# Kernel optimization log

Hardware: AMD Instinct MI355X
Metric: run time of the kernel (lower is better)

## Reference

```python
import jax, jax.numpy as jnp
import numpy as np

B, T, TM = 4, 1024, 1500
D_MODEL, D_FFN, H, D_HEAD, D_MEM = 1024, 4096, 16, 64, 1024
EPS = 1e-5


def layernorm(x, g):
    m = jnp.mean(x, axis=-1, keepdims=True)
    xc = x - m
    v = jnp.mean(xc * xc, axis=-1, keepdims=True)
    return xc * jax.lax.rsqrt(v + EPS) * g


def setup_inputs() -> dict:
    key = jax.random.key(0)
    ks = jax.random.split(key, 12)
    s = lambda fan_in: 1.0 / np.sqrt(fan_in)
    return {
        "x": jax.random.normal(ks[0], (B, T, D_MODEL), jnp.float32),
        "encoder_output": jax.random.normal(ks[1], (B, TM, D_MEM), jnp.float32),
        "encoder_mask": jax.random.randint(ks[2], (B, TM), 0, 2).astype(bool),
        "w_qkv": jax.random.normal(ks[3], (D_MODEL, 3 * H * D_HEAD), jnp.float32) * s(D_MODEL),
        "w_o_sa": jax.random.normal(ks[4], (H * D_HEAD, D_MODEL), jnp.float32) * s(H * D_HEAD),
        "w_q": jax.random.normal(ks[5], (D_MODEL, H * D_HEAD), jnp.float32) * s(D_MODEL),
        "w_kv": jax.random.normal(ks[6], (D_MEM, 2 * H * D_HEAD), jnp.float32) * s(D_MEM),
        "w_o_xa": jax.random.normal(ks[7], (H * D_HEAD, D_MODEL), jnp.float32) * s(H * D_HEAD),
        "w_ff1": jax.random.normal(ks[8], (D_MODEL, D_FFN), jnp.float32) * s(D_MODEL),
        "w_ff2": jax.random.normal(ks[9], (D_FFN, D_MODEL), jnp.float32) * s(D_FFN),
        "g_sa": jnp.ones((D_MODEL,), jnp.float32),
        "g_xaq": jnp.ones((D_MODEL,), jnp.float32),
        "g_xam": jnp.ones((D_MEM,), jnp.float32),
        "g_ff": jnp.ones((D_MODEL,), jnp.float32),
    }


def reference(x, encoder_output, encoder_mask, w_qkv, w_o_sa, w_q, w_kv, w_o_xa,
              w_ff1, w_ff2, g_sa, g_xaq, g_xam, g_ff):
    b, t, _ = x.shape
    scale = D_HEAD ** -0.5

    # ---- causal self-attention ----
    residual = x
    xn = layernorm(x, g_sa)
    qkv = (xn @ w_qkv).reshape(b, t, 3, H, D_HEAD)
    q, k, v = qkv[:, :, 0], qkv[:, :, 1], qkv[:, :, 2]  # (B,T,H,D)
    scores = jnp.einsum('bqhd,bkhd->bhqk', q, k) * scale
    causal = jnp.tril(jnp.ones((t, t), x.dtype))
    scores = scores + (1.0 - causal) * -1e9
    attn = jax.nn.softmax(scores, axis=-1)
    sa = jnp.einsum('bhqk,bkhd->bqhd', attn, v).reshape(b, t, H * D_HEAD)
    x = residual + sa @ w_o_sa

    # ---- cross-attention ----
    residual = x
    qn = layernorm(x, g_xaq)
    mn = layernorm(encoder_output, g_xam)
    tq, tm = t, mn.shape[1]
    qx = (qn @ w_q).reshape(b, tq, H, D_HEAD)
    kvx = (mn @ w_kv).reshape(b, tm, 2, H, D_HEAD)
    kx, vx = kvx[:, :, 0], kvx[:, :, 1]
    xs = jnp.einsum('bqhd,bkhd->bhqk', qx, kx) * scale
    xs = jnp.where(encoder_mask[:, None, None, :], xs, -jnp.inf)
    xattn = jax.nn.softmax(xs, axis=-1)
    xa = jnp.einsum('bhqk,bkhd->bqhd', xattn, vx).reshape(b, tq, H * D_HEAD)
    x = residual + xa @ w_o_xa

    # ---- pointwise FFN (kernel_size=1 conv == linear) ----
    residual = x
    h = layernorm(x, g_ff)
    h = jax.nn.gelu(h @ w_ff1, approximate=True) @ w_ff2
    x = residual + h
    return (x, k, v)
```

## Files before the change

kernel.cpp:

```cpp
#include <hip/hip_runtime.h>
#include <hip/hip_bf16.h>
#include <cstdint>
#include <cstddef>


typedef __attribute__((ext_vector_type(4))) float f32x4;
typedef __attribute__((ext_vector_type(8))) short s8v;
typedef __attribute__((ext_vector_type(2))) unsigned uint2v;

#define DEVI __device__ __forceinline__

DEVI short f2bf(float f) {
  union { float f; unsigned u; } x; x.f = f;
  unsigned r = x.u + 0x7fffu + ((x.u >> 16) & 1u);
  return (short)(r >> 16);
}
DEVI unsigned cvtpk_bf2(float lo, float hi) {
  unsigned r;
  asm("v_cvt_pk_bf16_f32 %0, %1, %2" : "=v"(r) : "v"(lo), "v"(hi));
  return r;
}
DEVI float fexp2(float x) {
  float r;
  asm("v_exp_f32 %0, %1" : "=v"(r) : "v"(x));
  return r;
}
DEVI float fmax3(float a, float b, float c) {
  float r;
  asm("v_max3_f32 %0, %1, %2, %3" : "=v"(r) : "v"(a), "v"(b), "v"(c));
  return r;
}
DEVI float bpermf(int srclane, float v) {
  union { float f; int i; } x; x.f = v;
  x.i = __builtin_amdgcn_ds_bpermute(srclane << 2, x.i);
  return x.f;
}
DEVI void gload_lds16(const void* g, void* l) {
  __builtin_amdgcn_global_load_lds((const __attribute__((address_space(1))) void*)g,
                                   (__attribute__((address_space(3))) void*)l,
                                   16, 0, 0);
}

DEVI void xcd_swizzle(int& bx, int& by) {
  int gx = gridDim.x, gy = gridDim.y;
  int nxy = gx * gy, chunk = nxy >> 3;
  int orig = blockIdx.y * gx + blockIdx.x;
  int gid = (orig & 7) * chunk + (orig >> 3);
  int full = gy << 3, nfull = gx >> 3, lim = nfull * full;
  if (gid < lim) {
    int band = gid / full, r = gid - band * full;
    bx = (band << 3) + (r & 7);
    by = r >> 3;
  } else {
    int r = gid - lim, w = gx - (nfull << 3);
    bx = (nfull << 3) + r % w;
    by = r / w;
  }
}

__global__ __launch_bounds__(256) void k_prep(
    const float* __restrict__ wqkv, const float* __restrict__ wosa,
    const float* __restrict__ wq,   const float* __restrict__ wkv,
    const float* __restrict__ woxa, const float* __restrict__ wff1,
    const float* __restrict__ wff2,
    short* __restrict__ wqkv_t, short* __restrict__ wosa_t,
    short* __restrict__ wq_t,   short* __restrict__ wkv_t,
    short* __restrict__ woxa_t, short* __restrict__ wff1_t,
    short* __restrict__ wff2_t,
    const int* __restrict__ mask, unsigned long long* __restrict__ mbits) {
  int id = blockIdx.x;
  const float* w; short* wt; int K, N, tx, r;
  if (id < 3072)       { w = wqkv; wt = wqkv_t; K = 1024; N = 3072; tx = 96;  r = id; }
  else if (id < 4096)  { w = wosa; wt = wosa_t; K = 1024; N = 1024; tx = 32;  r = id - 3072; }
  else if (id < 5120)  { w = wq;   wt = wq_t;   K = 1024; N = 1024; tx = 32;  r = id - 4096; }
  else if (id < 7168)  { w = wkv;  wt = wkv_t;  K = 1024; N = 2048; tx = 64;  r = id - 5120; }
  else if (id < 8192)  { w = woxa; wt = woxa_t; K = 1024; N = 1024; tx = 32;  r = id - 7168; }
  else if (id < 12288) { w = wff1; wt = wff1_t; K = 1024; N = 4096; tx = 128; r = id - 8192; }
  else if (id < 16384) { w = wff2; wt = wff2_t; K = 4096; N = 1024; tx = 32;  r = id - 12288; }
  else {
    int t = threadIdx.x;
    if (t < 96) {
      int b = t / 24, wd = t % 24;
      unsigned long long v = 0;
      const int* mb = mask + (size_t)b * 1500;
      for (int j = 0; j < 64; j++) {
        int k = wd * 64 + j;
        if (k < 1500 && mb[k]) v |= (1ull << j);
      }
      mbits[b * 24 + wd] = v;
    }
    return;
  }
  __shared__ float tile[32][33];
  int n0 = (r % tx) * 32, k0 = (r / tx) * 32;
  int t = threadIdx.x;
  int row = t >> 3, c4 = (t & 7) * 4;
  *(f32x4*)&tile[row][c4] = *(const f32x4*)(w + (size_t)(k0 + row) * N + n0 + c4);
  __syncthreads();
  float v0 = tile[c4 + 0][row], v1 = tile[c4 + 1][row];
  float v2 = tile[c4 + 2][row], v3 = tile[c4 + 3][row];
  uint2v o = {cvtpk_bf2(v0, v1), cvtpk_bf2(v2, v3)};
  *(uint2v*)(wt + (size_t)(n0 + row) * K + k0 + c4) = o;
}

__global__ __launch_bounds__(256) void k_vtrans(
    const short* __restrict__ src, int srs, int coff,
    short* __restrict__ dst, int T, int Tp) {
  __shared__ short tile[32][72];
  int bh = blockIdx.y, b = bh >> 4, h = bh & 15;
  int t0 = blockIdx.x * 32;
  const short* sB = src + (size_t)b * T * srs + coff + h * 64;
  short* dB = dst + (size_t)bh * 64 * Tp;
  int t = threadIdx.x;
  int r = t >> 3, c = (t & 7) * 8;
  int tr = t0 + r; if (tr > T - 1) tr = T - 1;
  *(s8v*)&tile[r][c] = *(const s8v*)(sB + (size_t)tr * srs + c);
  __syncthreads();
  int d = t & 63, ch = t >> 6;
  s8v o;
#pragma unroll
  for (int j = 0; j < 8; j++) o[j] = tile[ch * 8 + j][d];
  *(s8v*)(dB + (size_t)d * Tp + t0 + ch * 8) = o;
}

__global__ __launch_bounds__(256) void k_ln2(
    const float* __restrict__ x, const float* __restrict__ gx,
    short* __restrict__ ox,
    const float* __restrict__ e, const float* __restrict__ ge,
    short* __restrict__ oe) {
  int id = blockIdx.x;
  const float* src; const float* g; short* dst; int row;
  if (id < 4096) { src = x; g = gx; dst = ox; row = id; }
  else           { src = e; g = ge; dst = oe; row = id - 4096; }
  const float* xr = src + (size_t)row * 1024;
  int t = threadIdx.x, wid = t >> 6, lane = t & 63;
  f32x4 v = ((const f32x4*)xr)[t];
  float s = v[0] + v[1] + v[2] + v[3];
#pragma unroll
  for (int m = 32; m >= 1; m >>= 1) s += __shfl_xor(s, m);
  __shared__ float red[4];
  if (lane == 0) red[wid] = s;
  __syncthreads();
  float mean = (red[0] + red[1] + red[2] + red[3]) * (1.f / 1024.f);
  float q = 0.f;
#pragma unroll
  for (int i = 0; i < 4; i++) { v[i] -= mean; q += v[i] * v[i]; }
#pragma unroll
  for (int m = 32; m >= 1; m >>= 1) q += __shfl_xor(q, m);
  __syncthreads();
  if (lane == 0) red[wid] = q;
  __syncthreads();
  float var = (red[0] + red[1] + red[2] + red[3]) * (1.f / 1024.f);
  float rs = rsqrtf(var + 1e-5f);
  f32x4 gv = ((const f32x4*)g)[t];
  uint2v w = {cvtpk_bf2(v[0] * rs * gv[0], v[1] * rs * gv[1]),
              cvtpk_bf2(v[2] * rs * gv[2], v[3] * rs * gv[3])};
  *(uint2v*)(dst + (size_t)row * 1024 + t * 4) = w;
}

__global__ __launch_bounds__(256) void k_ln(
    const float* __restrict__ x, const float* __restrict__ g,
    short* __restrict__ out) {
  int row = blockIdx.x;
  const float* xr = x + (size_t)row * 1024;
  int t = threadIdx.x, wid = t >> 6, lane = t & 63;
  f32x4 v = ((const f32x4*)xr)[t];
  float s = v[0] + v[1] + v[2] + v[3];
#pragma unroll
  for (int m = 32; m >= 1; m >>= 1) s += __shfl_xor(s, m);
  __shared__ float red[4];
  if (lane == 0) red[wid] = s;
  __syncthreads();
  float mean = (red[0] + red[1] + red[2] + red[3]) * (1.f / 1024.f);
  float q = 0.f;
#pragma unroll
  for (int i = 0; i < 4; i++) { v[i] -= mean; q += v[i] * v[i]; }
#pragma unroll
  for (int m = 32; m >= 1; m >>= 1) q += __shfl_xor(q, m);
  __syncthreads();
  if (lane == 0) red[wid] = q;
  __syncthreads();
  float var = (red[0] + red[1] + red[2] + red[3]) * (1.f / 1024.f);
  float rs = rsqrtf(var + 1e-5f);
  f32x4 gv = ((const f32x4*)g)[t];
  uint2v w = {cvtpk_bf2(v[0] * rs * gv[0], v[1] * rs * gv[1]),
              cvtpk_bf2(v[2] * rs * gv[2], v[3] * rs * gv[3])};
  *(uint2v*)(out + (size_t)row * 1024 + t * 4) = w;
}

template <bool GELU_, bool F32OUT, bool BF16OUT, bool KV>
__global__ __launch_bounds__(512) void k_gemm4(
    const short* __restrict__ A, const short* __restrict__ Bt,
    float* __restrict__ Cf, short* __restrict__ Cb,
    float* __restrict__ okv, int M, int N, int K, int lda, int ldb) {
  __shared__ short As[128 * 64];
  __shared__ short Bs[256 * 64];

  int bx, by;
  xcd_swizzle(bx, by);
  int am = bx * 128, bn = by * 256;

  int t = threadIdx.x, wid = t >> 6, lane = t & 63;
  int la = lane & 15, lb = lane >> 4;
  int wr = wid >> 2, wc = wid & 3;

  const short* gpA[2]; const short* gpB[4];
  int dofA[2], dofB[4];
#pragma unroll
  for (int l = 0; l < 2; l++) {
    int c = l * 512 + t;
    int row = c >> 3, g = c & 7;
    int ar = am + row; if (ar > M - 1) ar = M - 1;
    gpA[l] = A + (size_t)ar * lda + ((g ^ (row & 7)) << 3);
    dofA[l] = (l * 512 + wid * 64) * 8;
  }
#pragma unroll
  for (int l = 0; l < 4; l++) {
    int c = l * 512 + t;
    int row = c >> 3, g = c & 7;
    gpB[l] = Bt + (size_t)(bn + row) * ldb + ((g ^ (row & 7)) << 3);
    dofB[l] = (l * 512 + wid * 64) * 8;
  }

  int aOff[4], bOff[4];
#pragma unroll
  for (int m = 0; m < 4; m++) {
    int r = wr * 64 + m * 16 + la;
    aOff[m] = r * 64 + ((lb ^ (r & 7)) << 3);
  }
#pragma unroll
  for (int n = 0; n < 4; n++) {
    int r = wc * 64 + n * 16 + la;
    bOff[n] = r * 64 + ((lb ^ (r & 7)) << 3);
  }

  f32x4 acc[4][4];
#pragma unroll
  for (int m = 0; m < 4; m++)
#pragma unroll
    for (int n = 0; n < 4; n++) acc[m][n] = (f32x4){0.f, 0.f, 0.f, 0.f};

  int nk = K >> 6;
  for (int ks = 0; ks < nk; ++ks) {
#pragma unroll
    for (int l = 0; l < 2; l++) { gload_lds16(gpA[l], As + dofA[l]); gpA[l] += 64; }
#pragma unroll
    for (int l = 0; l < 4; l++) { gload_lds16(gpB[l], Bs + dofB[l]); gpB[l] += 64; }
    __syncthreads();
#pragma unroll
    for (int kk = 0; kk < 2; kk++) {
      s8v af[4], bfg[4];
#pragma unroll
      for (int m = 0; m < 4; m++)
        af[m] = *(const s8v*)(As + (aOff[m] ^ (kk << 5)));
#pragma unroll
      for (int n = 0; n < 4; n++)
        bfg[n] = *(const s8v*)(Bs + (bOff[n] ^ (kk << 5)));
#pragma unroll
      for (int m = 0; m < 4; m++)
#pragma unroll
        for (int n = 0; n < 4; n++)
          acc[m][n] = __builtin_amdgcn_mfma_f32_16x16x32_bf16(af[m], bfg[n], acc[m][n], 0, 0, 0);
    }
    __syncthreads();
  }

#pragma unroll
  for (int m = 0; m < 4; m++) {
    int rb = am + wr * 64 + m * 16 + lb * 4;
#pragma unroll
    for (int n = 0; n < 4; n++) {
      int col = bn + wc * 64 + n * 16 + la;
#pragma unroll
      for (int j = 0; j < 4; j++) {
        int r = rb + j;
        if (r < M) {
          float v = acc[m][n][j];
          if (GELU_) {
            float u = v;
            float y = 0.7978845608f * u * (1.f + 0.044715f * u * u);
            float e = fexp2(fminf(y * 2.88539008f, 80.f));
            float th = (e - 1.f) * __builtin_amdgcn_rcpf(e + 1.f);
            v = 0.5f * u * (1.f + th);
          }
          if (F32OUT) Cf[(size_t)r * N + col] = v;
          if (BF16OUT) Cb[(size_t)r * N + col] = f2bf(v);
          if (KV) {
            if (col >= 2048)
              okv[(size_t)4096 * 1024 + (size_t)r * 1024 + (col - 2048)] = v;
            else if (col >= 1024)
              okv[(size_t)r * 1024 + (col - 1024)] = v;
          }
        }
      }
    }
  }
}

template <bool RES, bool F32OUT, bool BF16OUT>
__global__ __launch_bounds__(256) void k_gemm5(
    const short* __restrict__ A, const short* __restrict__ Bt,
    float* __restrict__ Cf, short* __restrict__ Cb,
    const float* __restrict__ res, int M, int N, int K, int lda, int ldb) {
  __shared__ short As[128 * 64];
  __shared__ short Bs[64 * 64];

  int bx, by;
  xcd_swizzle(bx, by);
  int am = bx * 128, bn = by * 64;

  int t = threadIdx.x, wid = t >> 6, lane = t & 63;
  int la = lane & 15, lb = lane >> 4;
  int wr = wid >> 1, wc = wid & 1;

  const short* gpA[4]; const short* gpB[2];
  int dofA[4], dofB[2];
#pragma unroll
  for (int l = 0; l < 4; l++) {
    int cl = l * 256 + t;
    int row = cl >> 3, g = cl & 7;
    int ar = am + row; if (ar > M - 1) ar = M - 1;
    gpA[l] = A + (size_t)ar * lda + ((g ^ (row & 7)) << 3);
    dofA[l] = (l * 256 + wid * 64) * 8;
  }
#pragma unroll
  for (int l = 0; l < 2; l++) {
    int cl = l * 256 + t;
    int row = cl >> 3, g = cl & 7;
    gpB[l] = Bt + (size_t)(bn + row) * ldb + ((g ^ (row & 7)) << 3);
    dofB[l] = (l * 256 + wid * 64) * 8;
  }

  int aOff[4], bOff[2];
#pragma unroll
  for (int m = 0; m < 4; m++) {
    int r = wr * 64 + m * 16 + la;
    aOff[m] = r * 64 + ((lb ^ (r & 7)) << 3);
  }
#pragma unroll
  for (int n = 0; n < 2; n++) {
    int r = wc * 32 + n * 16 + la;
    bOff[n] = r * 64 + ((lb ^ (r & 7)) << 3);
  }

  f32x4 acc[4][2];
#pragma unroll
  for (int m = 0; m < 4; m++)
#pragma unroll
    for (int n = 0; n < 2; n++) acc[m][n] = (f32x4){0.f, 0.f, 0.f, 0.f};

  int nk = K >> 6;
  for (int ks = 0; ks < nk; ++ks) {
#pragma unroll
    for (int l = 0; l < 4; l++) { gload_lds16(gpA[l], As + dofA[l]); gpA[l] += 64; }
#pragma unroll
    for (int l = 0; l < 2; l++) { gload_lds16(gpB[l], Bs + dofB[l]); gpB[l] += 64; }
    __syncthreads();
#pragma unroll
    for (int kk = 0; kk < 2; kk++) {
      s8v af[4], bfg[2];
#pragma unroll
      for (int m = 0; m < 4; m++)
        af[m] = *(const s8v*)(As + (aOff[m] ^ (kk << 5)));
#pragma unroll
      for (int n = 0; n < 2; n++)
        bfg[n] = *(const s8v*)(Bs + (bOff[n] ^ (kk << 5)));
#pragma unroll
      for (int m = 0; m < 4; m++)
#pragma unroll
        for (int n = 0; n < 2; n++)
          acc[m][n] = __builtin_amdgcn_mfma_f32_16x16x32_bf16(af[m], bfg[n], acc[m][n], 0, 0, 0);
    }
    __syncthreads();
  }

#pragma unroll
  for (int m = 0; m < 4; m++) {
    int rb = am + wr * 64 + m * 16 + lb * 4;
#pragma unroll
    for (int n = 0; n < 2; n++) {
      int col = bn + wc * 32 + n * 16 + la;
#pragma unroll
      for (int j = 0; j < 4; j++) {
        int r = rb + j;
        if (r < M) {
          float v = acc[m][n][j];
          if (RES) v += res[(size_t)r * N + col];
          if (F32OUT) Cf[(size_t)r * N + col] = v;
          if (BF16OUT) Cb[(size_t)r * N + col] = f2bf(v);
        }
      }
    }
  }
}

template <bool CAUSAL>
__global__ __launch_bounds__(512) void k_attn4(
    const short* __restrict__ qbuf, int qrs,
    const short* __restrict__ kbuf, int krs,
    const short* __restrict__ vT, int vts,
    short* __restrict__ obuf, int ors,
    const unsigned long long* __restrict__ mbits, int mwords,
    int Tq, int Tk, float scale) {
  __shared__ short Ks[64 * 64];
  __shared__ short Vs[64 * 64];
  __shared__ short Ps[8 * 1024];
  int lid = blockIdx.y * gridDim.x + blockIdx.x;
  int rest = lid >> 3;
  int bh = (lid & 7) * 8 + (rest & 7);
  int qsel = rest >> 3;
  int st = CAUSAL ? (7 - qsel) : qsel;
  int b = bh >> 4, h = bh & 15;
  int t = threadIdx.x, wid = t >> 6, lane = t & 63;
  int la = lane & 15, lb = lane >> 4;
  float lscale = scale * 1.44269504f;

  const short* qB = qbuf + (size_t)b * Tq * qrs + h * 64;
  const short* kB = kbuf + (size_t)b * Tk * krs + h * 64;
  const short* vB = vT + (size_t)bh * 64 * vts;
  char* Pw = (char*)(Ps + wid * 1024);

  int sr = t >> 3, scol = (t & 7) * 8;
  int swz = sr * 64 + (scol ^ ((sr & 7) << 3));

  int q0 = st * 128 + wid * 16;
  int nkt = CAUSAL ? 2 * st + 2 : (Tk + 63) >> 6;
  int lastkt = CAUSAL ? (q0 >> 6) : nkt - 1;

  s8v qf[2];
#pragma unroll
  for (int kk = 0; kk < 2; kk++)
    qf[kk] = *(const s8v*)(qB + (size_t)(q0 + la) * qrs + kk * 32 + lb * 8);

  f32x4 accO[4];
#pragma unroll
  for (int n = 0; n < 4; n++) accO[n] = (f32x4){0.f, 0.f, 0.f, 0.f};
  float m = -1e30f, l = 0.f;

  s8v krg, vrg;
  {
    int tk = sr; if (tk > Tk - 1) tk = Tk - 1;
    krg = *(const s8v*)(kB + (size_t)tk * krs + scol);
    vrg = *(const s8v*)(vB + (size_t)sr * vts + scol);
  }

  for (int kt = 0; kt < nkt; kt++) {
    int kb0 = kt << 6;
    __syncthreads();
    *(s8v*)&Ks[swz] = krg;
    *(s8v*)&Vs[swz] = vrg;
    __syncthreads();
    if (kt + 1 < nkt) {
      int kb = kb0 + 64;
      int tk = kb + sr; if (tk > Tk - 1) tk = Tk - 1;
      krg = *(const s8v*)(kB + (size_t)tk * krs + scol);
      vrg = *(const s8v*)(vB + (size_t)sr * vts + kb + scol);
    }
    if (kt > lastkt) continue;

    bool needMask;
    unsigned long long wm = ~0ull;
    if (CAUSAL) {
      needMask = (kt == lastkt);
    } else {
      wm = mbits[(size_t)b * mwords + kt];
      needMask = (wm != ~0ull);
    }

    float sc[4][4];
    __builtin_amdgcn_s_setprio(1);
#pragma unroll
    for (int n = 0; n < 4; n++) {
      f32x4 a = (f32x4){0.f, 0.f, 0.f, 0.f};
#pragma unroll
      for (int kk = 0; kk < 2; kk++) {
        s8v kf = *(const s8v*)&Ks[(n * 16 + la) * 64 +
                                  ((kk * 32 + lb * 8) ^ ((la & 7) << 3))];
        a = __builtin_amdgcn_mfma_f32_16x16x32_bf16(kf, qf[kk], a, 0, 0, 0);
      }
      if (needMask) {
#pragma unroll
        for (int j = 0; j < 4; j++) {
          int ki = n * 16 + lb * 4 + j;
          bool ok = CAUSAL ? (kb0 + ki <= q0 + la) : (((wm >> ki) & 1ull) != 0);
          sc[n][j] = ok ? a[j] : -1e30f;
        }
      } else {
#pragma unroll
        for (int j = 0; j < 4; j++) sc[n][j] = a[j];
      }
    }
    __builtin_amdgcn_s_setprio(0);

    float rn[4];
#pragma unroll
    for (int n = 0; n < 4; n++)
      rn[n] = fmaxf(fmax3(sc[n][0], sc[n][1], sc[n][2]), sc[n][3]);
    float tm = fmaxf(fmax3(rn[0], rn[1], rn[2]), rn[3]);
    tm = fmaxf(tm, __shfl_xor(tm, 16));
    tm = fmaxf(tm, __shfl_xor(tm, 32));
    tm = fmaxf(tm * lscale, -1e4f);

    bool skip = __all(tm - m <= 10.f);
    float alpha = 1.f;
    if (!skip) {
      float mn_ = fmaxf(m, tm);
      alpha = fexp2(m - mn_);
      m = mn_;
    }
    float nm = -m;

    unsigned W[4][2];
    float ps = 0.f;
#pragma unroll
    for (int n = 0; n < 4; n++) {
      float p0 = fexp2(__builtin_fmaf(sc[n][0], lscale, nm));
      float p1 = fexp2(__builtin_fmaf(sc[n][1], lscale, nm));
      float p2 = fexp2(__builtin_fmaf(sc[n][2], lscale, nm));
      float p3 = fexp2(__builtin_fmaf(sc[n][3], lscale, nm));
      ps += (p0 + p1) + (p2 + p3);
      W[n][0] = cvtpk_bf2(p0, p1);
      W[n][1] = cvtpk_bf2(p2, p3);
    }
    ps += __shfl_xor(ps, 16);
    ps += __shfl_xor(ps, 32);
    l = l * alpha + ps;

    if (!skip) {
#pragma unroll
      for (int j = 0; j < 4; j++) {
        float aj = bpermf(lb * 20 + j, alpha);
#pragma unroll
        for (int n = 0; n < 4; n++) accO[n][j] *= aj;
      }
    }

#pragma unroll
    for (int n = 0; n < 4; n++) {
      uint2v w2 = {W[n][0], W[n][1]};
      *(uint2v*)(Pw + ((la * 128 + n * 32 + lb * 8) ^ ((la & 7) << 4))) = w2;
    }
    __builtin_amdgcn_s_setprio(1);
#pragma unroll
    for (int kk = 0; kk < 2; kk++) {
      s8v pa = *(const s8v*)(Pw + ((la * 128 + kk * 64 + lb * 16) ^ ((la & 7) << 4)));
#pragma unroll
      for (int n = 0; n < 4; n++) {
        s8v vf = *(const s8v*)&Vs[(n * 16 + la) * 64 +
                                  ((kk * 32 + lb * 8) ^ ((la & 7) << 3))];
        accO[n] = __builtin_amdgcn_mfma_f32_16x16x32_bf16(pa, vf, accO[n], 0, 0, 0);
      }
    }
    __builtin_amdgcn_s_setprio(0);
  }

#pragma unroll
  for (int j = 0; j < 4; j++) {
    float lj = bpermf(lb * 20 + j, l);
    float inv = 1.f / lj;
    int r = q0 + lb * 4 + j;
#pragma unroll
    for (int n = 0; n < 4; n++)
      obuf[(size_t)(b * Tq + r) * ors + h * 64 + n * 16 + la] = f2bf(accO[n][j] * inv);
  }
}

extern "C" void kernel_launch(void* const* d_in, const int* in_sizes, int n_in,
                              void* d_out, int out_size, void* d_ws, size_t ws_size,
                              hipStream_t stream) {
  (void)in_sizes; (void)n_in; (void)out_size; (void)ws_size;
  const float* x      = (const float*)d_in[0];
  const float* enc    = (const float*)d_in[1];
  const int*   mask   = (const int*)d_in[2];
  const float* w_qkv  = (const float*)d_in[3];
  const float* w_o_sa = (const float*)d_in[4];
  const float* w_q    = (const float*)d_in[5];
  const float* w_kv   = (const float*)d_in[6];
  const float* w_o_xa = (const float*)d_in[7];
  const float* w_ff1  = (const float*)d_in[8];
  const float* w_ff2  = (const float*)d_in[9];
  const float* g_sa   = (const float*)d_in[10];
  const float* g_xaq  = (const float*)d_in[11];
  const float* g_xam  = (const float*)d_in[12];
  const float* g_ff   = (const float*)d_in[13];

  float* out_x = (float*)d_out;
  float* out_k = out_x + (size_t)4096 * 1024;

  char* ws = (char*)d_ws;
  size_t off = 0;
  auto alloc = [&](size_t bytes) -> void* {
    void* p = ws + off;
    off += (bytes + 255) & ~(size_t)255;
    return p;
  };
  short* wqkv_t = (short*)alloc((size_t)3072 * 1024 * 2);
  short* wosa_t = (short*)alloc((size_t)1024 * 1024 * 2);
  short* wq_t   = (short*)alloc((size_t)1024 * 1024 * 2);
  short* wkv_t  = (short*)alloc((size_t)2048 * 1024 * 2);
  short* woxa_t = (short*)alloc((size_t)1024 * 1024 * 2);
  short* wff1_t = (short*)alloc((size_t)4096 * 1024 * 2);
  short* wff2_t = (short*)alloc((size_t)1024 * 4096 * 2);
  short* xn     = (short*)alloc((size_t)4096 * 1024 * 2);
  short* qkv_b  = (short*)alloc((size_t)4096 * 3072 * 2);
  short* sa_b   = (short*)alloc((size_t)4096 * 1024 * 2);
  float* x1     = (float*)alloc((size_t)4096 * 1024 * 4);
  short* qn     = (short*)alloc((size_t)4096 * 1024 * 2);
  short* mn     = (short*)alloc((size_t)6000 * 1024 * 2);
  short* qx_b   = (short*)alloc((size_t)4096 * 1024 * 2);
  short* kvx_b  = (short*)alloc((size_t)6000 * 2048 * 2);
  short* xa_b   = (short*)alloc((size_t)4096 * 1024 * 2);
  float* x2     = (float*)alloc((size_t)4096 * 1024 * 4);
  short* hn     = (short*)alloc((size_t)4096 * 1024 * 2);
  short* h1     = (short*)alloc((size_t)4096 * 4096 * 2);
  unsigned long long* mbits = (unsigned long long*)alloc(4 * 24 * 8);

  short* vTsa = xn;
  short* vTxa = h1;

  k_prep<<<16385, 256, 0, stream>>>(
      w_qkv, w_o_sa, w_q, w_kv, w_o_xa, w_ff1, w_ff2,
      wqkv_t, wosa_t, wq_t, wkv_t, woxa_t, wff1_t, wff2_t, mask, mbits);
  k_ln2<<<10096, 256, 0, stream>>>(x, g_sa, xn, enc, g_xam, mn);

  k_gemm4<false, false, true, true><<<dim3(32, 12), 512, 0, stream>>>(
      xn, wqkv_t, nullptr, qkv_b, out_k, 4096, 3072, 1024, 1024, 1024);
  k_vtrans<<<dim3(32, 64), 256, 0, stream>>>(qkv_b, 3072, 2048, vTsa, 1024, 1024);
  k_attn4<true><<<dim3(8, 64), 512, 0, stream>>>(
      qkv_b, 3072, qkv_b + 1024, 3072, vTsa, 1024,
      sa_b, 1024, nullptr, 0, 1024, 1024, 0.125f);
  k_gemm5<true, true, false><<<dim3(32, 16), 256, 0, stream>>>(
      sa_b, wosa_t, x1, nullptr, x, 4096, 1024, 1024, 1024, 1024);
  k_ln<<<4096, 256, 0, stream>>>(x1, g_xaq, qn);

  k_gemm5<false, false, true><<<dim3(32, 16), 256, 0, stream>>>(
      qn, wq_t, nullptr, qx_b, nullptr, 4096, 1024, 1024, 1024, 1024);
  k_gemm4<false, false, true, false><<<dim3(47, 8), 512, 0, stream>>>(
      mn, wkv_t, nullptr, kvx_b, nullptr, 6000, 2048, 1024, 1024, 1024);
  k_vtrans<<<dim3(48, 64), 256, 0, stream>>>(kvx_b, 2048, 1024, vTxa, 1500, 1536);
  k_attn4<false><<<dim3(8, 64), 512, 0, stream>>>(
      qx_b, 1024, kvx_b, 2048, vTxa, 1536,
      xa_b, 1024, mbits, 24, 1024, 1500, 0.125f);
  k_gemm5<true, true, false><<<dim3(32, 16), 256, 0, stream>>>(
      xa_b, woxa_t, x2, nullptr, x1, 4096, 1024, 1024, 1024, 1024);
  k_ln<<<4096, 256, 0, stream>>>(x2, g_ff, hn);

  k_gemm4<true, false, true, false><<<dim3(32, 16), 512, 0, stream>>>(
      hn, wff1_t, nullptr, h1, nullptr, 4096, 4096, 1024, 1024, 1024);
  k_gemm5<true, true, false><<<dim3(32, 16), 256, 0, stream>>>(
      h1, wff2_t, out_x, nullptr, x2, 4096, 1024, 4096, 4096, 4096);
}
```

Before: 387.6 us.

## Split-K the FFN down-projection GEMM with a separate residual reduction kernel

The final FFN2 GEMM (K=4096, N=1024) previously ran on k_gemm5 with a 32x16 grid. It now uses k_gemm4 with a split-K of 4 along blockIdx.z, each slice writing fp32 partials into the reused qkv buffer. A new vectorised kernel sums the four partials plus the residual into the output. This trades extra fp32 partial traffic (about 64 MB written and read) and one more launch for more blocks and shorter K loops per block.

```diff
diff --git a/kernel.cpp b/kernel.cpp
--- a/kernel.cpp
+++ b/kernel.cpp
@@ -188,13 +188,19 @@
   *(uint2v*)(out + (size_t)row * 1024 + t * 4) = w;
 }
 
-template <bool GELU_, bool F32OUT, bool BF16OUT, bool KV>
+template <bool GELU_, bool F32OUT, bool BF16OUT, bool KV, bool SPLIT>
 __global__ __launch_bounds__(512) void k_gemm4(
     const short* __restrict__ A, const short* __restrict__ Bt,
     float* __restrict__ Cf, short* __restrict__ Cb,
     float* __restrict__ okv, int M, int N, int K, int lda, int ldb) {
   __shared__ short As[128 * 64];
   __shared__ short Bs[256 * 64];
+  if (SPLIT) {
+    int z = blockIdx.z;
+    A += (size_t)z * K;
+    Bt += (size_t)z * K;
+    if (F32OUT) Cf += (size_t)z * (size_t)M * N;
+  }
 
   int bx, by;
   xcd_swizzle(bx, by);
@@ -392,6 +398,15 @@
       }
     }
   }
+}
+
+__global__ __launch_bounds__(256) void k_red4(
+    const f32x4* __restrict__ p, const f32x4* __restrict__ res,
+    float* __restrict__ outf, int n) {
+  int i = blockIdx.x * 256 + threadIdx.x;
+  f32x4 v = res[i] + ((p[i] + p[i + (size_t)n]) +
+                      (p[i + 2 * (size_t)n] + p[i + 3 * (size_t)n]));
+  ((f32x4*)outf)[i] = v;
 }
 
 template <bool CAUSAL>
@@ -617,13 +632,15 @@
 
   short* vTsa = xn;
   short* vTxa = h1;
+  float* partQ = (float*)qkv_b;
+  const int NRED = 1048576;
 
   k_prep<<<16385, 256, 0, stream>>>(
       w_qkv, w_o_sa, w_q, w_kv, w_o_xa, w_ff1, w_ff2,
       wqkv_t, wosa_t, wq_t, wkv_t, woxa_t, wff1_t, wff2_t, mask, mbits);
   k_ln2<<<10096, 256, 0, stream>>>(x, g_sa, xn, enc, g_xam, mn);
 
-  k_gemm4<false, false, true, true><<<dim3(32, 12), 512, 0, stream>>>(
+  k_gemm4<false, false, true, true, false><<<dim3(32, 12), 512, 0, stream>>>(
       xn, wqkv_t, nullptr, qkv_b, out_k, 4096, 3072, 1024, 1024, 1024);
   k_vtrans<<<dim3(32, 64), 256, 0, stream>>>(qkv_b, 3072, 2048, vTsa, 1024, 1024);
   k_attn4<true><<<dim3(8, 64), 512, 0, stream>>>(
@@ -635,7 +652,7 @@
 
   k_gemm5<false, false, true><<<dim3(32, 16), 256, 0, stream>>>(
       qn, wq_t, nullptr, qx_b, nullptr, 4096, 1024, 1024, 1024, 1024);
-  k_gemm4<false, false, true, false><<<dim3(47, 8), 512, 0, stream>>>(
+  k_gemm4<false, false, true, false, false><<<dim3(47, 8), 512, 0, stream>>>(
       mn, wkv_t, nullptr, kvx_b, nullptr, 6000, 2048, 1024, 1024, 1024);
   k_vtrans<<<dim3(48, 64), 256, 0, stream>>>(kvx_b, 2048, 1024, vTxa, 1500, 1536);
   k_attn4<false><<<dim3(8, 64), 512, 0, stream>>>(
@@ -645,8 +662,10 @@
       xa_b, woxa_t, x2, nullptr, x1, 4096, 1024, 1024, 1024, 1024);
   k_ln<<<4096, 256, 0, stream>>>(x2, g_ff, hn);
 
-  k_gemm4<true, false, true, false><<<dim3(32, 16), 512, 0, stream>>>(
+  k_gemm4<true, false, true, false, false><<<dim3(32, 16), 512, 0, stream>>>(
       hn, wff1_t, nullptr, h1, nullptr, 4096, 4096, 1024, 1024, 1024);
-  k_gemm5<true, true, false><<<dim3(32, 16), 256, 0, stream>>>(
-      h1, wff2_t, out_x, nullptr, x2, 4096, 1024, 4096, 4096, 4096);
-}
+  k_gemm4<false, true, false, false, true><<<dim3(32, 4, 4), 512, 0, stream>>>(
+      h1, wff2_t, partQ, nullptr, nullptr, 4096, 1024, 1024, 4096, 4096);
+  k_red4<<<4096, 256, 0, stream>>>(
+      (const f32x4*)partQ, (const f32x4*)x2, out_x, NRED);
+}
```

Result: no change. 384.2 us (-0.9%).
